# Kernel optimization log

Hardware: AMD Instinct MI355X
Metric: run time of the kernel (lower is better)

Reference implementation:

```python
import jax, jax.numpy as jnp
import numpy as np

S, D, E = 8192, 2048, 64
CAPACITY_FACTOR = 1.0
MIN_CAPACITY = 4
CAPACITY = max(int(np.ceil(S / E * CAPACITY_FACTOR)), MIN_CAPACITY)  # 128


def setup_inputs() -> dict:
    key = jax.random.key(0)
    kx, kw = jax.random.split(key)
    x = jax.random.normal(kx, (S, D), dtype=jnp.float32)
    wg = jax.random.normal(kw, (D, E), dtype=jnp.float32) * (1.0 / np.sqrt(D))
    return {"x": x, "wg": wg}


def reference(x, wg):
    # logits from the gate's linear projection: [S, E]
    logits = x @ wg
    gates = jax.nn.softmax(logits, axis=1)  # token_sel_expert_weights

    # top-1 expert per token
    idx = jnp.argmax(gates, axis=1)  # [S]
    mask1 = jax.nn.one_hot(idx, E, dtype=jnp.int32)  # [S, E]

    # load-balancing auxiliary loss
    me = jnp.mean(gates, axis=0)
    ce = jnp.mean(mask1.astype(gates.dtype), axis=0)
    l_aux = jnp.sum(me * ce) * E

    # capacity drop: keep first CAPACITY tokens per expert
    # torch.topk(mask, k=C, dim=0) on a 0/1 mask -> earliest C selected tokens per expert
    _, top_idx = jax.lax.top_k(mask1.T, CAPACITY)  # [E, C] token indices
    keep = jnp.zeros((S, E), jnp.int32).at[top_idx, jnp.arange(E)[:, None]].set(1)
    mask1 = mask1 * keep

    gates_masked = gates * mask1.astype(gates.dtype)  # [S, E]

    # position of each kept token within its expert
    locations = jnp.cumsum(mask1, axis=0) - 1  # [S, E]
    offsets = jnp.sum(locations * mask1, axis=1)  # [S], 0 for dropped tokens

    # combine weights [S, E, C] and dispatch mask
    loc_sc = jax.nn.one_hot(offsets, CAPACITY, dtype=gates.dtype)  # [S, C]
    combine_weights = jnp.einsum('se,sc->sec', gates_masked, loc_sc)
    dispatch_mask = combine_weights > 0
    return l_aux, combine_weights, dispatch_mask
```

## Files before the change

kernel.cpp:

```cpp
#include <hip/hip_runtime.h>
#include <hip/hip_bf16.h>

#define SS 8192
#define DD 2048
#define EE 64
#define CAP 128
#define SEC (67108864LL)

typedef float floatx4 __attribute__((ext_vector_type(4)));

__device__ __forceinline__ float bcast(float v, int lane) {
    return __builtin_bit_cast(float,
        __builtin_amdgcn_readlane(__builtin_bit_cast(int, v), lane));
}

__global__ __launch_bounds__(256) void k_fill_gate(const float* __restrict__ x,
                                                   const float* __restrict__ wg,
                                                   float* __restrict__ out,
                                                   int* __restrict__ idx_out,
                                                   float* __restrict__ gval_out,
                                                   float* __restrict__ gpart) {
    if (blockIdx.x >= 512) {
        const int fb = blockIdx.x - 512;
        floatx4* __restrict__ out4 = (floatx4*)out;
        const size_t base = (size_t)fb * 4096 + threadIdx.x;
        const floatx4 z = {0.f, 0.f, 0.f, 0.f};
#pragma unroll
        for (int k = 0; k < 16; ++k)
            __builtin_nontemporal_store(z, &out4[base + (size_t)k * 256]);
        if (fb == 0 && threadIdx.x == 0) out[2 * SEC] = 0.f;
        return;
    }

    const int bid = blockIdx.x;
    const int lane = threadIdx.x & 63;
    const int wv = __builtin_amdgcn_readfirstlane(threadIdx.x >> 6);
    const int tg = wv >> 1;
    const int dh = wv & 1;
    const int tokBase = bid * 16 + tg * 8;
    const float* xp = x + (size_t)tokBase * DD + dh * 1024;
    const float* wp = wg + (size_t)dh * 1024 * EE + lane;

    float acc[8] = {0.f, 0.f, 0.f, 0.f, 0.f, 0.f, 0.f, 0.f};

    for (int b = 0; b < 16; ++b) {
        float xv[8];
#pragma unroll
        for (int t = 0; t < 8; ++t)
            xv[t] = xp[(size_t)t * DD + b * 64 + lane];

#pragma unroll
        for (int g = 0; g < 4; ++g) {
            float w[16];
#pragma unroll
            for (int j = 0; j < 16; ++j)
                w[j] = wp[(size_t)(b * 64 + g * 16 + j) * EE];
#pragma unroll
            for (int j = 0; j < 16; ++j) {
#pragma unroll
                for (int t = 0; t < 8; ++t)
                    acc[t] = fmaf(bcast(xv[t], g * 16 + j), w[j], acc[t]);
            }
        }
    }

    __shared__ float part[4][8][64];
#pragma unroll
    for (int t = 0; t < 8; ++t) part[wv][t][lane] = acc[t];
    __syncthreads();

    __shared__ float gshare[2][64];
    if (dh == 0) {
        float gs = 0.f;
#pragma unroll
        for (int t = 0; t < 8; ++t) {
            float v = part[wv][t][lane] + part[wv + 1][t][lane];
            float m = v;
            int mi = lane;
#pragma unroll
            for (int off = 1; off < 64; off <<= 1) {
                float ov = __shfl_xor(m, off);
                int oi = __shfl_xor(mi, off);
                if (ov > m || (ov == m && oi < mi)) { m = ov; mi = oi; }
            }
            float p = __expf(v - m);
            float s = p;
#pragma unroll
            for (int off = 1; off < 64; off <<= 1) s += __shfl_xor(s, off);
            gs += p / s;
            if (lane == 0) {
                idx_out[tokBase + t] = mi;
                gval_out[tokBase + t] = 1.0f / s;
            }
        }
        gshare[tg][lane] = gs;
    }
    __syncthreads();
    if (wv == 0) {
        gpart[(size_t)bid * 64 + lane] = gshare[0][lane] + gshare[1][lane];
    }
}

__global__ __launch_bounds__(256) void k_scatter(const int* __restrict__ idx,
                                                 const float* __restrict__ gval,
                                                 float* __restrict__ out,
                                                 int* __restrict__ counts) {
    const int e = blockIdx.x;
    const int tid = threadIdx.x;
    const int lane = tid & 63;
    const int wv = tid >> 6;

    __shared__ int wtot[4];
    int running = 0;

    for (int s0 = 0; s0 < SS; s0 += 256) {
        const int s = s0 + tid;
        const bool flag = (idx[s] == e);
        unsigned long long mask = __ballot(flag);
        int excl = __popcll(mask & ((1ULL << lane) - 1ULL));
        int wt = __popcll(mask);
        if (lane == 0) wtot[wv] = wt;
        __syncthreads();
        int pre = 0;
#pragma unroll
        for (int w2 = 0; w2 < 4; ++w2)
            if (w2 < wv) pre += wtot[w2];
        const int blockTot = wtot[0] + wtot[1] + wtot[2] + wtot[3];
        const int rank = running + pre + excl;
        if (flag && rank < CAP) {
            const size_t o = (size_t)s * (EE * CAP) + (size_t)e * CAP + rank;
            out[1 + o] = gval[s];
            out[1 + (size_t)SEC + o] = 1.0f;
        }
        running += blockTot;
        __syncthreads();
    }
    if (tid == 0) counts[e] = running;
}

__global__ __launch_bounds__(1024) void k_laux(const float* __restrict__ gpart,
                                               const int* __restrict__ counts,
                                               float* __restrict__ out) {
    const int lane = threadIdx.x & 63;
    const int stripe = threadIdx.x >> 6;
    float s = 0.f;
    for (int b = stripe; b < 512; b += 16) s += gpart[(size_t)b * 64 + lane];
    __shared__ float red[16][64];
    red[stripe][lane] = s;
    __syncthreads();
    if (threadIdx.x < 64) {
        float gsum = 0.f;
#pragma unroll
        for (int r = 0; r < 16; ++r) gsum += red[r][lane];
        float term = gsum * (float)counts[lane];
#pragma unroll
        for (int off = 1; off < 64; off <<= 1) term += __shfl_xor(term, off);
        if (lane == 0)
            out[0] = term * ((float)EE / ((float)SS * (float)SS));
    }
}

extern "C" void kernel_launch(void* const* d_in, const int* in_sizes, int n_in,
                              void* d_out, int out_size, void* d_ws, size_t ws_size,
                              hipStream_t stream) {
    const float* x = (const float*)d_in[0];
    const float* wg = (const float*)d_in[1];
    float* out = (float*)d_out;

    int* idxp = (int*)d_ws;
    float* gval = (float*)d_ws + SS;
    float* gpart = (float*)d_ws + 2 * SS;
    int* counts = (int*)d_ws + 2 * SS + 512 * 64;

    hipLaunchKernelGGL(k_fill_gate, dim3(8704), dim3(256), 0, stream,
                       x, wg, out, idxp, gval, gpart);
    hipLaunchKernelGGL(k_scatter, dim3(64), dim3(256), 0, stream, idxp, gval, out, counts);
    hipLaunchKernelGGL(k_laux, dim3(1), dim3(1024), 0, stream, gpart, counts, out);
}
```

Before: 162.0 us.

## Fuse scatter and aux-loss kernels, one wave per expert without block syncs

Merges the scatter and l_aux kernels into a single launch of 17 blocks. In the first 16 blocks each wave handles one expert on its own and computes ranks with ballot/popcount, which removes the per-chunk __syncthreads. The last block rebuilds the expert counts with a shared-memory atomic histogram and computes the aux loss at the same time, removing one launch and the dependency on counts. Each wave now scans all 8192 tokens serially with 64-wide steps, giving less parallelism per expert, and the l_aux block does redundant histogram work.

```diff
diff --git a/kernel.cpp b/kernel.cpp
--- a/kernel.cpp
+++ b/kernel.cpp
@@ -101,58 +101,46 @@
     }
 }
 
-__global__ __launch_bounds__(256) void k_scatter(const int* __restrict__ idx,
-                                                 const float* __restrict__ gval,
-                                                 float* __restrict__ out,
-                                                 int* __restrict__ counts) {
-    const int e = blockIdx.x;
+__global__ __launch_bounds__(256) void k_scatter_laux(const int* __restrict__ idx,
+                                                      const float* __restrict__ gval,
+                                                      const float* __restrict__ gpart,
+                                                      float* __restrict__ out) {
     const int tid = threadIdx.x;
     const int lane = tid & 63;
     const int wv = tid >> 6;
 
-    __shared__ int wtot[4];
-    int running = 0;
+    if (blockIdx.x < 16) {
+        const int e = blockIdx.x * 4 + wv;
+        int running = 0;
+        for (int c = 0; c < 128; ++c) {
+            const int s = c * 64 + lane;
+            const bool flag = (idx[s] == e);
+            const unsigned long long mask = __ballot(flag);
+            const int rank = running + __popcll(mask & ((1ULL << lane) - 1ULL));
+            if (flag && rank < CAP) {
+                const size_t o = (size_t)s * (EE * CAP) + (size_t)e * CAP + rank;
+                out[1 + o] = gval[s];
+                out[1 + (size_t)SEC + o] = 1.0f;
+            }
+            running += __popcll(mask);
+        }
+        return;
+    }
 
-    for (int s0 = 0; s0 < SS; s0 += 256) {
-        const int s = s0 + tid;
-        const bool flag = (idx[s] == e);
-        unsigned long long mask = __ballot(flag);
-        int excl = __popcll(mask & ((1ULL << lane) - 1ULL));
-        int wt = __popcll(mask);
-        if (lane == 0) wtot[wv] = wt;
-        __syncthreads();
-        int pre = 0;
-#pragma unroll
-        for (int w2 = 0; w2 < 4; ++w2)
-            if (w2 < wv) pre += wtot[w2];
-        const int blockTot = wtot[0] + wtot[1] + wtot[2] + wtot[3];
-        const int rank = running + pre + excl;
-        if (flag && rank < CAP) {
-            const size_t o = (size_t)s * (EE * CAP) + (size_t)e * CAP + rank;
-            out[1 + o] = gval[s];
-            out[1 + (size_t)SEC + o] = 1.0f;
-        }
-        running += blockTot;
-        __syncthreads();
-    }
-    if (tid == 0) counts[e] = running;
-}
+    __shared__ int hist[64];
+    if (tid < 64) hist[tid] = 0;
+    __syncthreads();
+    for (int s = tid; s < SS; s += 256) atomicAdd(&hist[idx[s]], 1);
+    __syncthreads();
 
-__global__ __launch_bounds__(1024) void k_laux(const float* __restrict__ gpart,
-                                               const int* __restrict__ counts,
-                                               float* __restrict__ out) {
-    const int lane = threadIdx.x & 63;
-    const int stripe = threadIdx.x >> 6;
-    float s = 0.f;
-    for (int b = stripe; b < 512; b += 16) s += gpart[(size_t)b * 64 + lane];
-    __shared__ float red[16][64];
-    red[stripe][lane] = s;
+    float sum = 0.f;
+    for (int b = wv; b < 512; b += 4) sum += gpart[(size_t)b * 64 + lane];
+    __shared__ float red[4][64];
+    red[wv][lane] = sum;
     __syncthreads();
-    if (threadIdx.x < 64) {
-        float gsum = 0.f;
-#pragma unroll
-        for (int r = 0; r < 16; ++r) gsum += red[r][lane];
-        float term = gsum * (float)counts[lane];
+    if (tid < 64) {
+        float gsum = red[0][lane] + red[1][lane] + red[2][lane] + red[3][lane];
+        float term = gsum * (float)hist[lane];
 #pragma unroll
         for (int off = 1; off < 64; off <<= 1) term += __shfl_xor(term, off);
         if (lane == 0)
@@ -170,10 +158,9 @@
     int* idxp = (int*)d_ws;
     float* gval = (float*)d_ws + SS;
     float* gpart = (float*)d_ws + 2 * SS;
-    int* counts = (int*)d_ws + 2 * SS + 512 * 64;
 
     hipLaunchKernelGGL(k_fill_gate, dim3(8704), dim3(256), 0, stream,
                        x, wg, out, idxp, gval, gpart);
-    hipLaunchKernelGGL(k_scatter, dim3(64), dim3(256), 0, stream, idxp, gval, out, counts);
-    hipLaunchKernelGGL(k_laux, dim3(1), dim3(1024), 0, stream, gpart, counts, out);
+    hipLaunchKernelGGL(k_scatter_laux, dim3(17), dim3(256), 0, stream,
+                       idxp, gval, gpart, out);
 }
```

Result: slower. 175.5 us (+8.3%).
